# Performance work log

Measured on AMD Instinct MI355X. Metric: run time of the kernel, lower is better.

## Reference

```python
import jax, jax.numpy as jnp
import numpy as np

# Static configuration matching init_kwargs
LR_SHAPES = ((64, 64), (128, 128), (256, 256))
H0, W0 = LR_SHAPES[0]          # selected layer (layer_number = 0)
UP = (8, 8)                     # upscale factors -> output_dim = 64
OUT_DIM = UP[0] * UP[1]
KERNEL = (3, 3)
PAD = (1, 1)
BATCH = 64
WEIGHTS_IN = 189                # 9 + 36 + 144


def _unfold(x, kernel, stride, pad):
    """torch.F.unfold equivalent for NCHW input with C==1.
    x: (N, 1, H, W) -> (N, kh*kw, L) with row-major spatial positions."""
    patches = jax.lax.conv_general_dilated_patches(
        x,
        filter_shape=kernel,
        window_strides=stride,
        padding=((pad[0], pad[0]), (pad[1], pad[1])),
        dimension_numbers=('NCHW', 'OIHW', 'NCHW'),
    )  # (N, kh*kw, H_out, W_out)
    n, k, h, w = patches.shape
    return patches.reshape(n, k, h * w)


def setup_inputs() -> dict:
    key = jax.random.key(0)
    k0, k1, k2, kw = jax.random.split(key, 4)
    x0 = jax.random.normal(k0, (BATCH, 1, 64, 64), dtype=jnp.float32)
    x1 = jax.random.normal(k1, (BATCH, 1, 128, 128), dtype=jnp.float32)
    x2 = jax.random.normal(k2, (BATCH, 1, 256, 256), dtype=jnp.float32)
    # original uses uniform(-stdv, stdv) with tiny stdv; small-scale normal keeps
    # the softmax non-degenerate while matching the magnitude regime
    weight = jax.random.normal(kw, (WEIGHTS_IN, OUT_DIM), dtype=jnp.float32) * 0.01
    return {"x0": x0, "x1": x1, "x2": x2, "weight": weight}


def reference(x0, x1, x2, weight):
    xs = (x0, x1, x2)
    cols = []
    for j, (hj, wj) in enumerate(LR_SHAPES):
        s = (hj // H0, wj // W0)                       # scale vs selected layer
        f = (KERNEL[0] * s[0], KERNEL[1] * s[1])       # scaled kernel
        p = (PAD[0] * s[0], PAD[1] * s[1])             # scaled padding
        cols.append(_unfold(xs[j], f, s, p))           # (N, 9*s0*s1, L)
    X = jnp.concatenate(cols, axis=1)                  # (N, 189, L), L = H0*W0

    # per-pixel attention weights: matmul + ReLU + softmax
    logits = jax.nn.relu(jnp.einsum('nkl,ko->nlo', X, weight))  # (N, L, 64)
    soft = jax.nn.softmax(logits, axis=-1)                       # (N, L, 64)

    # reassemble: each LR pixel value scaled by its 64 attention weights (C==1)
    xsel = x0.reshape(x0.shape[0], H0 * W0)            # (N, L)
    out = xsel[:, :, None] * soft                      # (N, L, 64)

    # fold(kernel=1) == reshape to (N, 64, H0, W0)
    n = out.shape[0]
    out = out.transpose(0, 2, 1).reshape(n, OUT_DIM, H0, W0)

    # pixel shuffle -> (N, 1, H0*up0, W0*up1)
    out = out.reshape(n, 1, UP[0], UP[1], H0, W0)
    out = out.transpose(0, 1, 4, 2, 5, 3)
    return out.reshape(n, 1, H0 * UP[0], W0 * UP[1])
```

## Files before the change

### kernel.cpp

```cpp
#include <hip/hip_runtime.h>

typedef _Float16 f16;
typedef f16 f16x8 __attribute__((ext_vector_type(8)));
typedef f16 f16x4 __attribute__((ext_vector_type(4)));
typedef float f32x4 __attribute__((ext_vector_type(4)));

#define S0 28
#define S1 48
#define S2 92
#define T0OFF 0
#define T1OFF (11 * S0)
#define T2OFF (T1OFF + 20 * S1)
#define TILEH (T2OFF + 40 * S2)
#define LOG2E 1.4426950408889634f

__global__ void prep_wt(const float* __restrict__ W, f16* __restrict__ Wt) {
  const int f = blockIdx.x * 256 + threadIdx.x;
  const int s = f >> 8;
  const int t = (f >> 6) & 3;
  const int lane = f & 63;
  const int quad = lane >> 4, ln = lane & 15;
  const int n = t * 16 + ln;
  f16 vals[8];
  #pragma unroll
  for (int j = 0; j < 8; ++j) {
    int kp = s * 32 + quad * 8 + j;
    int orig = -1;
    if (kp < 16)      { int ki = kp >> 2, kj = kp & 3;                   if (ki < 3 && kj < 3) orig = 3*ki + kj; }
    else if (kp < 64) { int kk = kp - 16; int ki = kk >> 3, kj = kk & 7;  if (kj < 6)          orig = 9 + 6*ki + kj; }
    else              { int kk = kp - 64; int ki = kk >> 4, kj = kk & 15; if (kj < 12)         orig = 45 + 12*ki + kj; }
    vals[j] = (f16)((orig >= 0) ? W[orig * 64 + n] : 0.f);
  }
  *(f16x8*)(Wt + (size_t)f * 8) = *(const f16x8*)vals;
}

__global__ __launch_bounds__(256, 8) void fuse_kernel(
    const float* __restrict__ x0, const float* __restrict__ x1,
    const float* __restrict__ x2, const f16* __restrict__ Wt,
    float* __restrict__ out)
{
  __shared__ __align__(16) f16 tiles[TILEH];

  const int tid  = threadIdx.x;
  const int bid  = ((blockIdx.x & 7) << 8) | (blockIdx.x >> 3);
  const int nb   = bid >> 5;
  const int ty   = (bid >> 2) & 7;
  const int tx   = bid & 3;
  const int lane = tid & 63;
  const int wid  = tid >> 6;
  const int ln   = lane & 15;
  const int quad = lane >> 4;

  const f16* __restrict__ wfrag = Wt + (size_t)lane * 8;

  f32x4 v2[4];
  {
    const float* img = x2 + nb * 65536;
    #pragma unroll
    for (int i = 0; i < 4; ++i) {
      int idx = tid + 256 * i;
      int r  = idx / 22, c4 = idx - r * 22;
      int gy = ty * 32 - 4 + r;
      int gx = tx * 64 - 8 + 4 * c4;
      bool inb = (i < 3 || tid < 112) && ((unsigned)gy < 256u) && ((unsigned)gx < 256u);
      v2[i] = inb ? *(const f32x4*)(img + gy * 256 + gx) : (f32x4){0.f, 0.f, 0.f, 0.f};
    }
  }

  {
    const float* img = x1 + nb * 16384;
    int idx = tid;
    int r  = idx / 11, c4 = idx - r * 11;
    int gy = ty * 16 - 2 + r;
    int gx = tx * 32 - 4 + 4 * c4;
    bool inb = (idx < 220) && ((unsigned)gy < 128u) && ((unsigned)gx < 128u);
    f32x4 t = inb ? *(const f32x4*)(img + gy * 128 + gx) : (f32x4){0.f, 0.f, 0.f, 0.f};
    if (idx < 220) {
      f16x4 h; h[0] = (f16)t[0]; h[1] = (f16)t[1]; h[2] = (f16)t[2]; h[3] = (f16)t[3];
      *(f16x4*)&tiles[T1OFF + r * S1 + 4 * c4] = h;
    }
  }
  {
    const float* img = x0 + nb * 4096;
    int idx = tid;
    int r  = idx / 6, c4 = idx - r * 6;
    int gy = ty * 8 - 1 + r;
    int gx = tx * 16 - 4 + 4 * c4;
    bool inb = (idx < 66) && ((unsigned)gy < 64u) && ((unsigned)gx < 64u);
    f32x4 t = inb ? *(const f32x4*)(img + gy * 64 + gx) : (f32x4){0.f, 0.f, 0.f, 0.f};
    if (idx < 66) {
      f16x4 h; h[0] = (f16)t[0]; h[1] = (f16)t[1]; h[2] = (f16)t[2]; h[3] = (f16)t[3];
      *(f16x4*)&tiles[T0OFF + r * S0 + 4 * c4] = h;
    }
  }

  float xs[2];
  #pragma unroll
  for (int cc = 0; cc < 2; ++cc)
    xs[cc] = x0[nb * 4096 + (ty * 8 + wid * 2 + cc) * 64 + tx * 16 + ln];

  #pragma unroll
  for (int i = 0; i < 4; ++i) {
    if (i < 3 || tid < 112) {
      int idx = tid + 256 * i;
      int r  = idx / 22, c4 = idx - r * 22;
      f16x4 h; h[0] = (f16)v2[i][0]; h[1] = (f16)v2[i][1];
      h[2] = (f16)v2[i][2]; h[3] = (f16)v2[i][3];
      *(f16x4*)&tiles[T2OFF + r * S2 + 4 * c4] = h;
    }
  }

  f16x8 bf0[4];
  #pragma unroll
  for (int t = 0; t < 4; ++t)
    bf0[t] = *(const f16x8*)(wfrag + t * 512);

  __syncthreads();

  f32x4 acc[2][4];
  #pragma unroll
  for (int c = 0; c < 2; ++c)
    #pragma unroll
    for (int t = 0; t < 4; ++t)
      acc[c][t] = (f32x4){0.f, 0.f, 0.f, 0.f};

  {
    #pragma unroll
    for (int cc = 0; cc < 2; ++cc) {
      const int py = wid * 2 + cc;
      f16x8 a;
      if (quad < 2) {
        const int a0 = T0OFF + (py + 2 * quad) * S0 + ln + 3;
        #pragma unroll
        for (int j = 0; j < 4; ++j) a[j]     = tiles[a0 + j];
        #pragma unroll
        for (int j = 0; j < 4; ++j) a[4 + j] = tiles[a0 + S0 + j];
      } else {
        const int a1 = T1OFF + (2 * py + quad - 2) * S1 + 2 * ln + 2;
        #pragma unroll
        for (int j = 0; j < 8; ++j) a[j] = tiles[a1 + j];
      }
      #pragma unroll
      for (int t = 0; t < 4; ++t)
        acc[cc][t] = __builtin_amdgcn_mfma_f32_16x16x32_f16(bf0[t], a, acc[cc][t], 0, 0, 0);
    }
  }
  {
    f16x8 bf[4];
    #pragma unroll
    for (int t = 0; t < 4; ++t)
      bf[t] = *(const f16x8*)(wfrag + (4 + t) * 512);
    #pragma unroll
    for (int cc = 0; cc < 2; ++cc) {
      const int py = wid * 2 + cc;
      const int a1 = T1OFF + (2 * py + 2 + quad) * S1 + 2 * ln + 2;
      f16x8 a;
      #pragma unroll
      for (int j = 0; j < 8; ++j) a[j] = tiles[a1 + j];
      #pragma unroll
      for (int t = 0; t < 4; ++t)
        acc[cc][t] = __builtin_amdgcn_mfma_f32_16x16x32_f16(bf[t], a, acc[cc][t], 0, 0, 0);
    }
  }
  #pragma unroll 3
  for (int s = 2; s < 8; ++s) {
    f16x8 bf[4];
    #pragma unroll
    for (int t = 0; t < 4; ++t)
      bf[t] = *(const f16x8*)(wfrag + (s * 4 + t) * 512);
    #pragma unroll
    for (int cc = 0; cc < 2; ++cc) {
      const int py = wid * 2 + cc;
      const int b2 = T2OFF + (4 * py + 2 * (s - 2) + (quad >> 1)) * S2 + 4 * ln + 4 + 8 * (quad & 1);
      f16x4 lo = *(const f16x4*)&tiles[b2];
      f16x4 hi = *(const f16x4*)&tiles[b2 + 4];
      f16x8 a;
      a[0] = lo[0]; a[1] = lo[1]; a[2] = lo[2]; a[3] = lo[3];
      a[4] = hi[0]; a[5] = hi[1]; a[6] = hi[2]; a[7] = hi[3];
      #pragma unroll
      for (int t = 0; t < 4; ++t)
        acc[cc][t] = __builtin_amdgcn_mfma_f32_16x16x32_f16(bf[t], a, acc[cc][t], 0, 0, 0);
    }
  }

  const int gx8 = (tx * 16 + ln) * 8;
  #pragma unroll
  for (int cc = 0; cc < 2; ++cc) {
    float v[4][4];
    float m = 0.f;
    #pragma unroll
    for (int t = 0; t < 4; ++t)
      #pragma unroll
      for (int r = 0; r < 4; ++r) {
        float x = fmaxf(acc[cc][t][r], 0.f);
        v[t][r] = x;
        m = fmaxf(m, x);
      }
    m = fmaxf(m, __shfl_xor(m, 16));
    m = fmaxf(m, __shfl_xor(m, 32));

    float sden = 0.f;
    #pragma unroll
    for (int t = 0; t < 4; ++t)
      #pragma unroll
      for (int r = 0; r < 4; ++r) {
        float e = exp2f((v[t][r] - m) * LOG2E);
        v[t][r] = e;
        sden += e;
      }
    sden += __shfl_xor(sden, 16);
    sden += __shfl_xor(sden, 32);

    const float sc = xs[cc] * __builtin_amdgcn_rcpf(sden);
    const int gy = ty * 8 + wid * 2 + cc;
    float* op = out + nb * 262144 + (gy * 8 + (quad >> 1)) * 512 + gx8 + 4 * (quad & 1);
    #pragma unroll
    for (int t = 0; t < 4; ++t) {
      f32x4 w;
      w[0] = v[t][0] * sc; w[1] = v[t][1] * sc;
      w[2] = v[t][2] * sc; w[3] = v[t][3] * sc;
      __builtin_nontemporal_store(w, (f32x4*)(op + t * 1024));
    }
  }
}

extern "C" void kernel_launch(void* const* d_in, const int* in_sizes, int n_in,
                              void* d_out, int out_size, void* d_ws, size_t ws_size,
                              hipStream_t stream) {
  const float* x0 = (const float*)d_in[0];
  const float* x1 = (const float*)d_in[1];
  const float* x2 = (const float*)d_in[2];
  const float* W  = (const float*)d_in[3];
  float* outp     = (float*)d_out;
  f16* Wt         = (f16*)d_ws;

  prep_wt<<<dim3(8), dim3(256), 0, stream>>>(W, Wt);
  fuse_kernel<<<dim3(2048), dim3(256), 0, stream>>>(x0, x1, x2, Wt, outp);
}
```

Baseline: 124.1 us.

## Process two tiles per block with double-buffered LDS to overlap loads and compute

Each block now handles two horizontally adjacent tiles using two LDS buffers. The global loads for the second tile are issued before the first tile's MFMA loop and committed to LDS afterwards, so memory latency overlaps compute and the epilogue stores. The grid is halved and launch bounds drop from 8 to 6 blocks per CU. This costs more LDS and registers per block and fewer resident waves, and the barrier now waits only on LDS counters.

```diff
diff --git a/kernel.cpp b/kernel.cpp
--- a/kernel.cpp
+++ b/kernel.cpp
@@ -12,6 +12,7 @@
 #define T1OFF (11 * S0)
 #define T2OFF (T1OFF + 20 * S1)
 #define TILEH (T2OFF + 40 * S2)
+#define TILEP 4952
 #define LOG2E 1.4426950408889634f
 
 __global__ void prep_wt(const float* __restrict__ W, f16* __restrict__ Wt) {
@@ -34,90 +35,61 @@
   *(f16x8*)(Wt + (size_t)f * 8) = *(const f16x8*)vals;
 }
 
-__global__ __launch_bounds__(256, 8) void fuse_kernel(
-    const float* __restrict__ x0, const float* __restrict__ x1,
-    const float* __restrict__ x2, const f16* __restrict__ Wt,
-    float* __restrict__ out)
-{
-  __shared__ __align__(16) f16 tiles[TILEH];
-
-  const int tid  = threadIdx.x;
-  const int bid  = ((blockIdx.x & 7) << 8) | (blockIdx.x >> 3);
-  const int nb   = bid >> 5;
-  const int ty   = (bid >> 2) & 7;
-  const int tx   = bid & 3;
-  const int lane = tid & 63;
-  const int wid  = tid >> 6;
-  const int ln   = lane & 15;
-  const int quad = lane >> 4;
-
-  const f16* __restrict__ wfrag = Wt + (size_t)lane * 8;
-
-  f32x4 v2[4];
-  {
-    const float* img = x2 + nb * 65536;
-    #pragma unroll
-    for (int i = 0; i < 4; ++i) {
-      int idx = tid + 256 * i;
-      int r  = idx / 22, c4 = idx - r * 22;
-      int gy = ty * 32 - 4 + r;
-      int gx = tx * 64 - 8 + 4 * c4;
-      bool inb = (i < 3 || tid < 112) && ((unsigned)gy < 256u) && ((unsigned)gx < 256u);
-      v2[i] = inb ? *(const f32x4*)(img + gy * 256 + gx) : (f32x4){0.f, 0.f, 0.f, 0.f};
-    }
-  }
-
-  {
-    const float* img = x1 + nb * 16384;
-    int idx = tid;
-    int r  = idx / 11, c4 = idx - r * 11;
-    int gy = ty * 16 - 2 + r;
-    int gx = tx * 32 - 4 + 4 * c4;
-    bool inb = (idx < 220) && ((unsigned)gy < 128u) && ((unsigned)gx < 128u);
-    f32x4 t = inb ? *(const f32x4*)(img + gy * 128 + gx) : (f32x4){0.f, 0.f, 0.f, 0.f};
-    if (idx < 220) {
-      f16x4 h; h[0] = (f16)t[0]; h[1] = (f16)t[1]; h[2] = (f16)t[2]; h[3] = (f16)t[3];
-      *(f16x4*)&tiles[T1OFF + r * S1 + 4 * c4] = h;
-    }
-  }
-  {
-    const float* img = x0 + nb * 4096;
-    int idx = tid;
-    int r  = idx / 6, c4 = idx - r * 6;
-    int gy = ty * 8 - 1 + r;
-    int gx = tx * 16 - 4 + 4 * c4;
-    bool inb = (idx < 66) && ((unsigned)gy < 64u) && ((unsigned)gx < 64u);
-    f32x4 t = inb ? *(const f32x4*)(img + gy * 64 + gx) : (f32x4){0.f, 0.f, 0.f, 0.f};
-    if (idx < 66) {
-      f16x4 h; h[0] = (f16)t[0]; h[1] = (f16)t[1]; h[2] = (f16)t[2]; h[3] = (f16)t[3];
-      *(f16x4*)&tiles[T0OFF + r * S0 + 4 * c4] = h;
-    }
-  }
-
-  float xs[2];
-  #pragma unroll
-  for (int cc = 0; cc < 2; ++cc)
-    xs[cc] = x0[nb * 4096 + (ty * 8 + wid * 2 + cc) * 64 + tx * 16 + ln];
-
+__device__ __forceinline__ void issue_x2(const float* __restrict__ img, int ty, int tx,
+                                         int tid, f32x4 v[4]) {
+  #pragma unroll
+  for (int i = 0; i < 4; ++i) {
+    int idx = tid + 256 * i;
+    int r  = idx / 22, c4 = idx - r * 22;
+    int gy = ty * 32 - 4 + r;
+    int gx = tx * 64 - 8 + 4 * c4;
+    bool inb = (i < 3 || tid < 112) && ((unsigned)gy < 256u) && ((unsigned)gx < 256u);
+    v[i] = inb ? *(const f32x4*)(img + gy * 256 + gx) : (f32x4){0.f, 0.f, 0.f, 0.f};
+  }
+}
+
+__device__ __forceinline__ void commit_x2(f16* buf, int tid, const f32x4 v[4]) {
   #pragma unroll
   for (int i = 0; i < 4; ++i) {
     if (i < 3 || tid < 112) {
       int idx = tid + 256 * i;
       int r  = idx / 22, c4 = idx - r * 22;
-      f16x4 h; h[0] = (f16)v2[i][0]; h[1] = (f16)v2[i][1];
-      h[2] = (f16)v2[i][2]; h[3] = (f16)v2[i][3];
-      *(f16x4*)&tiles[T2OFF + r * S2 + 4 * c4] = h;
-    }
-  }
-
-  f16x8 bf0[4];
-  #pragma unroll
-  for (int t = 0; t < 4; ++t)
-    bf0[t] = *(const f16x8*)(wfrag + t * 512);
-
-  __syncthreads();
-
-  f32x4 acc[2][4];
+      f16x4 h; h[0] = (f16)v[i][0]; h[1] = (f16)v[i][1];
+      h[2] = (f16)v[i][2]; h[3] = (f16)v[i][3];
+      *(f16x4*)&buf[T2OFF + r * S2 + 4 * c4] = h;
+    }
+  }
+}
+
+__device__ __forceinline__ void stage_x1(const float* __restrict__ img, int ty, int tx,
+                                         int tid, f16* buf) {
+  int r  = tid / 11, c4 = tid - r * 11;
+  int gy = ty * 16 - 2 + r;
+  int gx = tx * 32 - 4 + 4 * c4;
+  bool inb = (tid < 220) && ((unsigned)gy < 128u) && ((unsigned)gx < 128u);
+  f32x4 t = inb ? *(const f32x4*)(img + gy * 128 + gx) : (f32x4){0.f, 0.f, 0.f, 0.f};
+  if (tid < 220) {
+    f16x4 h; h[0] = (f16)t[0]; h[1] = (f16)t[1]; h[2] = (f16)t[2]; h[3] = (f16)t[3];
+    *(f16x4*)&buf[T1OFF + r * S1 + 4 * c4] = h;
+  }
+}
+
+__device__ __forceinline__ void stage_x0(const float* __restrict__ img, int ty, int tx,
+                                         int tid, f16* buf) {
+  int r  = tid / 6, c4 = tid - r * 6;
+  int gy = ty * 8 - 1 + r;
+  int gx = tx * 16 - 4 + 4 * c4;
+  bool inb = (tid < 66) && ((unsigned)gy < 64u) && ((unsigned)gx < 64u);
+  f32x4 t = inb ? *(const f32x4*)(img + gy * 64 + gx) : (f32x4){0.f, 0.f, 0.f, 0.f};
+  if (tid < 66) {
+    f16x4 h; h[0] = (f16)t[0]; h[1] = (f16)t[1]; h[2] = (f16)t[2]; h[3] = (f16)t[3];
+    *(f16x4*)&buf[T0OFF + r * S0 + 4 * c4] = h;
+  }
+}
+
+__device__ __forceinline__ void kloop(const f16* buf, const f16* __restrict__ wfrag,
+                                      int wid, int ln, int quad,
+                                      const f16x8 bf0[4], f32x4 acc[2][4]) {
   #pragma unroll
   for (int c = 0; c < 2; ++c)
     #pragma unroll
@@ -132,13 +104,13 @@
       if (quad < 2) {
         const int a0 = T0OFF + (py + 2 * quad) * S0 + ln + 3;
         #pragma unroll
-        for (int j = 0; j < 4; ++j) a[j]     = tiles[a0 + j];
+        for (int j = 0; j < 4; ++j) a[j]     = buf[a0 + j];
         #pragma unroll
-        for (int j = 0; j < 4; ++j) a[4 + j] = tiles[a0 + S0 + j];
+        for (int j = 0; j < 4; ++j) a[4 + j] = buf[a0 + S0 + j];
       } else {
         const int a1 = T1OFF + (2 * py + quad - 2) * S1 + 2 * ln + 2;
         #pragma unroll
-        for (int j = 0; j < 8; ++j) a[j] = tiles[a1 + j];
+        for (int j = 0; j < 8; ++j) a[j] = buf[a1 + j];
       }
       #pragma unroll
       for (int t = 0; t < 4; ++t)
@@ -156,7 +128,7 @@
       const int a1 = T1OFF + (2 * py + 2 + quad) * S1 + 2 * ln + 2;
       f16x8 a;
       #pragma unroll
-      for (int j = 0; j < 8; ++j) a[j] = tiles[a1 + j];
+      for (int j = 0; j < 8; ++j) a[j] = buf[a1 + j];
       #pragma unroll
       for (int t = 0; t < 4; ++t)
         acc[cc][t] = __builtin_amdgcn_mfma_f32_16x16x32_f16(bf[t], a, acc[cc][t], 0, 0, 0);
@@ -172,8 +144,8 @@
     for (int cc = 0; cc < 2; ++cc) {
       const int py = wid * 2 + cc;
       const int b2 = T2OFF + (4 * py + 2 * (s - 2) + (quad >> 1)) * S2 + 4 * ln + 4 + 8 * (quad & 1);
-      f16x4 lo = *(const f16x4*)&tiles[b2];
-      f16x4 hi = *(const f16x4*)&tiles[b2 + 4];
+      f16x4 lo = *(const f16x4*)&buf[b2];
+      f16x4 hi = *(const f16x4*)&buf[b2 + 4];
       f16x8 a;
       a[0] = lo[0]; a[1] = lo[1]; a[2] = lo[2]; a[3] = lo[3];
       a[4] = hi[0]; a[5] = hi[1]; a[6] = hi[2]; a[7] = hi[3];
@@ -182,7 +154,11 @@
         acc[cc][t] = __builtin_amdgcn_mfma_f32_16x16x32_f16(bf[t], a, acc[cc][t], 0, 0, 0);
     }
   }
-
+}
+
+__device__ __forceinline__ void epilogue(const f32x4 acc[2][4], const float xs[2],
+                                         float* __restrict__ outnb, int ty, int tx,
+                                         int wid, int ln, int quad) {
   const int gx8 = (tx * 16 + ln) * 8;
   #pragma unroll
   for (int cc = 0; cc < 2; ++cc) {
@@ -213,7 +189,7 @@
 
     const float sc = xs[cc] * __builtin_amdgcn_rcpf(sden);
     const int gy = ty * 8 + wid * 2 + cc;
-    float* op = out + nb * 262144 + (gy * 8 + (quad >> 1)) * 512 + gx8 + 4 * (quad & 1);
+    float* op = outnb + (gy * 8 + (quad >> 1)) * 512 + gx8 + 4 * (quad & 1);
     #pragma unroll
     for (int t = 0; t < 4; ++t) {
       f32x4 w;
@@ -222,6 +198,83 @@
       __builtin_nontemporal_store(w, (f32x4*)(op + t * 1024));
     }
   }
+}
+
+#define BAR_LDS() do {                                        \
+    asm volatile("s_waitcnt lgkmcnt(0)" ::: "memory");        \
+    __builtin_amdgcn_s_barrier();                             \
+    asm volatile("" ::: "memory");                            \
+  } while (0)
+
+__global__ __launch_bounds__(256, 6) void fuse_kernel(
+    const float* __restrict__ x0, const float* __restrict__ x1,
+    const float* __restrict__ x2, const f16* __restrict__ Wt,
+    float* __restrict__ out)
+{
+  __shared__ __align__(16) f16 tiles[2 * TILEP];
+
+  const int tid  = threadIdx.x;
+  const int bid  = ((blockIdx.x & 7) << 7) | (blockIdx.x >> 3);
+  const int nb   = bid >> 4;
+  const int rem  = bid & 15;
+  const int ty   = rem >> 1;
+  const int tx0  = (rem & 1) << 1;
+  const int tx1  = tx0 + 1;
+  const int lane = tid & 63;
+  const int wid  = tid >> 6;
+  const int ln   = lane & 15;
+  const int quad = lane >> 4;
+
+  const f16* __restrict__ wfrag = Wt + (size_t)lane * 8;
+  const float* __restrict__ img0 = x0 + nb * 4096;
+  const float* __restrict__ img1 = x1 + nb * 16384;
+  const float* __restrict__ img2 = x2 + nb * 65536;
+  float* __restrict__ outnb = out + nb * 262144;
+  f16* buf0 = tiles;
+  f16* buf1 = tiles + TILEP;
+
+  f32x4 v2[4];
+  issue_x2(img2, ty, tx0, tid, v2);
+  stage_x1(img1, ty, tx0, tid, buf0);
+  stage_x0(img0, ty, tx0, tid, buf0);
+  float xs0[2];
+  #pragma unroll
+  for (int cc = 0; cc < 2; ++cc)
+    xs0[cc] = img0[(ty * 8 + wid * 2 + cc) * 64 + tx0 * 16 + ln];
+  commit_x2(buf0, tid, v2);
+
+  f32x4 v2b[4];
+  issue_x2(img2, ty, tx1, tid, v2b);
+
+  f16x8 bf0a[4];
+  #pragma unroll
+  for (int t = 0; t < 4; ++t)
+    bf0a[t] = *(const f16x8*)(wfrag + t * 512);
+
+  BAR_LDS();
+
+  f32x4 acc0[2][4];
+  kloop(buf0, wfrag, wid, ln, quad, bf0a, acc0);
+
+  commit_x2(buf1, tid, v2b);
+  stage_x1(img1, ty, tx1, tid, buf1);
+  stage_x0(img0, ty, tx1, tid, buf1);
+  float xs1[2];
+  #pragma unroll
+  for (int cc = 0; cc < 2; ++cc)
+    xs1[cc] = img0[(ty * 8 + wid * 2 + cc) * 64 + tx1 * 16 + ln];
+  f16x8 bf0b[4];
+  #pragma unroll
+  for (int t = 0; t < 4; ++t)
+    bf0b[t] = *(const f16x8*)(wfrag + t * 512);
+
+  epilogue(acc0, xs0, outnb, ty, tx0, wid, ln, quad);
+
+  BAR_LDS();
+
+  f32x4 acc1[2][4];
+  kloop(buf1, wfrag, wid, ln, quad, bf0b, acc1);
+  epilogue(acc1, xs1, outnb, ty, tx1, wid, ln, quad);
 }
 
 extern "C" void kernel_launch(void* const* d_in, const int* in_sizes, int n_in,
@@ -235,5 +288,5 @@
   f16* Wt         = (f16*)d_ws;
 
   prep_wt<<<dim3(8), dim3(256), 0, stream>>>(W, Wt);
-  fuse_kernel<<<dim3(2048), dim3(256), 0, stream>>>(x0, x1, x2, Wt, outp);
-}
+  fuse_kernel<<<dim3(1024), dim3(256), 0, stream>>>(x0, x1, x2, Wt, outp);
+}
```

New measurement: 135.2 us. 8.9% more time.

## Load x2 halo tile directly into LDS via global_load_lds as fp32

Applied to the files above, without the earlier changes.

Replaces the register-staged fp32 load, fp16 conversion and LDS store of the x2 halo tile with asynchronous global_load_lds transfers that write fp32 straight into shared memory. Out-of-bounds addresses are clamped and those slots zeroed after the first barrier, and conversion to fp16 moves into the MFMA operand build. This cuts VGPR pressure and instruction count in the prologue. In exchange LDS use roughly doubles for the x2 tile, so the occupancy hint drops from 8 to 6 blocks, and each inner-loop read now needs conversion instructions.

```diff
diff --git a/kernel.cpp b/kernel.cpp
--- a/kernel.cpp
+++ b/kernel.cpp
@@ -7,11 +7,10 @@
 
 #define S0 28
 #define S1 48
-#define S2 92
 #define T0OFF 0
 #define T1OFF (11 * S0)
-#define T2OFF (T1OFF + 20 * S1)
-#define TILEH (T2OFF + 40 * S2)
+#define T01N  (T1OFF + 20 * S1)
+#define X2N   3520
 #define LOG2E 1.4426950408889634f
 
 __global__ void prep_wt(const float* __restrict__ W, f16* __restrict__ Wt) {
@@ -34,12 +33,25 @@
   *(f16x8*)(Wt + (size_t)f * 8) = *(const f16x8*)vals;
 }
 
-__global__ __launch_bounds__(256, 8) void fuse_kernel(
+__device__ __forceinline__ void gload_lds16(const float* g, float* l) {
+  __builtin_amdgcn_global_load_lds(
+      (const __attribute__((address_space(1))) unsigned int*)g,
+      (__attribute__((address_space(3))) unsigned int*)l, 16, 0, 0);
+}
+
+#define BAR_LDS() do {                                        \
+    asm volatile("s_waitcnt lgkmcnt(0)" ::: "memory");        \
+    __builtin_amdgcn_s_barrier();                             \
+    asm volatile("" ::: "memory");                            \
+  } while (0)
+
+__global__ __launch_bounds__(256, 6) void fuse_kernel(
     const float* __restrict__ x0, const float* __restrict__ x1,
     const float* __restrict__ x2, const f16* __restrict__ Wt,
     float* __restrict__ out)
 {
-  __shared__ __align__(16) f16 tiles[TILEH];
+  __shared__ __align__(16) f16   t01[T01N];
+  __shared__ __align__(16) float x2f[3584];
 
   const int tid  = threadIdx.x;
   const int bid  = ((blockIdx.x & 7) << 8) | (blockIdx.x >> 3);
@@ -52,45 +64,45 @@
   const int quad = lane >> 4;
 
   const f16* __restrict__ wfrag = Wt + (size_t)lane * 8;
-
-  f32x4 v2[4];
-  {
-    const float* img = x2 + nb * 65536;
-    #pragma unroll
-    for (int i = 0; i < 4; ++i) {
-      int idx = tid + 256 * i;
-      int r  = idx / 22, c4 = idx - r * 22;
-      int gy = ty * 32 - 4 + r;
-      int gx = tx * 64 - 8 + 4 * c4;
-      bool inb = (i < 3 || tid < 112) && ((unsigned)gy < 256u) && ((unsigned)gx < 256u);
-      v2[i] = inb ? *(const f32x4*)(img + gy * 256 + gx) : (f32x4){0.f, 0.f, 0.f, 0.f};
+  const float* __restrict__ img2 = x2 + nb * 65536;
+
+  #pragma unroll
+  for (int i = 0; i < 4; ++i) {
+    int idx = i * 4 + wid;
+    if (idx < 14) {
+      int e   = idx * 256 + lane * 4;
+      int row = e / 88;
+      int col = e - row * 88;
+      int gy  = ty * 32 - 4 + row;
+      int gx  = tx * 64 - 8 + col;
+      int gyc = gy < 0 ? 0 : (gy > 255 ? 255 : gy);
+      int gxc = gx < 0 ? 0 : (gx > 252 ? 252 : gx);
+      gload_lds16(img2 + gyc * 256 + gxc, x2f + idx * 256);
     }
   }
 
   {
     const float* img = x1 + nb * 16384;
-    int idx = tid;
-    int r  = idx / 11, c4 = idx - r * 11;
+    int r  = tid / 11, c4 = tid - r * 11;
     int gy = ty * 16 - 2 + r;
     int gx = tx * 32 - 4 + 4 * c4;
-    bool inb = (idx < 220) && ((unsigned)gy < 128u) && ((unsigned)gx < 128u);
+    bool inb = (tid < 220) && ((unsigned)gy < 128u) && ((unsigned)gx < 128u);
     f32x4 t = inb ? *(const f32x4*)(img + gy * 128 + gx) : (f32x4){0.f, 0.f, 0.f, 0.f};
-    if (idx < 220) {
+    if (tid < 220) {
       f16x4 h; h[0] = (f16)t[0]; h[1] = (f16)t[1]; h[2] = (f16)t[2]; h[3] = (f16)t[3];
-      *(f16x4*)&tiles[T1OFF + r * S1 + 4 * c4] = h;
+      *(f16x4*)&t01[T1OFF + r * S1 + 4 * c4] = h;
     }
   }
   {
     const float* img = x0 + nb * 4096;
-    int idx = tid;
-    int r  = idx / 6, c4 = idx - r * 6;
+    int r  = tid / 6, c4 = tid - r * 6;
     int gy = ty * 8 - 1 + r;
     int gx = tx * 16 - 4 + 4 * c4;
-    bool inb = (idx < 66) && ((unsigned)gy < 64u) && ((unsigned)gx < 64u);
+    bool inb = (tid < 66) && ((unsigned)gy < 64u) && ((unsigned)gx < 64u);
     f32x4 t = inb ? *(const f32x4*)(img + gy * 64 + gx) : (f32x4){0.f, 0.f, 0.f, 0.f};
-    if (idx < 66) {
+    if (tid < 66) {
       f16x4 h; h[0] = (f16)t[0]; h[1] = (f16)t[1]; h[2] = (f16)t[2]; h[3] = (f16)t[3];
-      *(f16x4*)&tiles[T0OFF + r * S0 + 4 * c4] = h;
+      *(f16x4*)&t01[T0OFF + r * S0 + 4 * c4] = h;
     }
   }
 
@@ -99,23 +111,28 @@
   for (int cc = 0; cc < 2; ++cc)
     xs[cc] = x0[nb * 4096 + (ty * 8 + wid * 2 + cc) * 64 + tx * 16 + ln];
 
-  #pragma unroll
-  for (int i = 0; i < 4; ++i) {
-    if (i < 3 || tid < 112) {
-      int idx = tid + 256 * i;
-      int r  = idx / 22, c4 = idx - r * 22;
-      f16x4 h; h[0] = (f16)v2[i][0]; h[1] = (f16)v2[i][1];
-      h[2] = (f16)v2[i][2]; h[3] = (f16)v2[i][3];
-      *(f16x4*)&tiles[T2OFF + r * S2 + 4 * c4] = h;
-    }
-  }
-
   f16x8 bf0[4];
   #pragma unroll
   for (int t = 0; t < 4; ++t)
     bf0[t] = *(const f16x8*)(wfrag + t * 512);
 
   __syncthreads();
+
+  #pragma unroll
+  for (int i = 0; i < 4; ++i) {
+    int idx = i * 4 + wid;
+    if (idx < 14) {
+      int e   = idx * 256 + lane * 4;
+      int row = e / 88;
+      int col = e - row * 88;
+      int gy  = ty * 32 - 4 + row;
+      int gx  = tx * 64 - 8 + col;
+      bool valid = (e < X2N) && ((unsigned)gy < 256u) && ((unsigned)gx <= 252u);
+      if (!valid && e < X2N)
+        *(f32x4*)&x2f[e] = (f32x4){0.f, 0.f, 0.f, 0.f};
+    }
+  }
+  BAR_LDS();
 
   f32x4 acc[2][4];
   #pragma unroll
@@ -132,13 +149,13 @@
       if (quad < 2) {
         const int a0 = T0OFF + (py + 2 * quad) * S0 + ln + 3;
         #pragma unroll
-        for (int j = 0; j < 4; ++j) a[j]     = tiles[a0 + j];
+        for (int j = 0; j < 4; ++j) a[j]     = t01[a0 + j];
         #pragma unroll
-        for (int j = 0; j < 4; ++j) a[4 + j] = tiles[a0 + S0 + j];
+        for (int j = 0; j < 4; ++j) a[4 + j] = t01[a0 + S0 + j];
       } else {
         const int a1 = T1OFF + (2 * py + quad - 2) * S1 + 2 * ln + 2;
         #pragma unroll
-        for (int j = 0; j < 8; ++j) a[j] = tiles[a1 + j];
+        for (int j = 0; j < 8; ++j) a[j] = t01[a1 + j];
       }
       #pragma unroll
       for (int t = 0; t < 4; ++t)
@@ -156,7 +173,7 @@
       const int a1 = T1OFF + (2 * py + 2 + quad) * S1 + 2 * ln + 2;
       f16x8 a;
       #pragma unroll
-      for (int j = 0; j < 8; ++j) a[j] = tiles[a1 + j];
+      for (int j = 0; j < 8; ++j) a[j] = t01[a1 + j];
       #pragma unroll
       for (int t = 0; t < 4; ++t)
         acc[cc][t] = __builtin_amdgcn_mfma_f32_16x16x32_f16(bf[t], a, acc[cc][t], 0, 0, 0);
@@ -171,12 +188,12 @@
     #pragma unroll
     for (int cc = 0; cc < 2; ++cc) {
       const int py = wid * 2 + cc;
-      const int b2 = T2OFF + (4 * py + 2 * (s - 2) + (quad >> 1)) * S2 + 4 * ln + 4 + 8 * (quad & 1);
-      f16x4 lo = *(const f16x4*)&tiles[b2];
-      f16x4 hi = *(const f16x4*)&tiles[b2 + 4];
+      const int b2 = (4 * py + 2 * (s - 2) + (quad >> 1)) * 88 + 4 * ln + 4 + 8 * (quad & 1);
+      f32x4 lo = *(const f32x4*)&x2f[b2];
+      f32x4 hi = *(const f32x4*)&x2f[b2 + 4];
       f16x8 a;
-      a[0] = lo[0]; a[1] = lo[1]; a[2] = lo[2]; a[3] = lo[3];
-      a[4] = hi[0]; a[5] = hi[1]; a[6] = hi[2]; a[7] = hi[3];
+      #pragma unroll
+      for (int j = 0; j < 4; ++j) { a[j] = (f16)lo[j]; a[4 + j] = (f16)hi[j]; }
       #pragma unroll
       for (int t = 0; t < 4; ++t)
         acc[cc][t] = __builtin_amdgcn_mfma_f32_16x16x32_f16(bf[t], a, acc[cc][t], 0, 0, 0);
```

New measurement: 112.0 us. 9.8% less time.
